# Optimization experiments

Measured on AMD Instinct MI355X. Metric: run time of the kernel, lower is better.

The kernel has to match this reference:

```python
import jax, jax.numpy as jnp
import numpy as np

B, S, D = 2, 2048, 1024
H = 16
HD = D // H  # 64
SCALE = HD ** -0.5
EPS = 1e-12  # F.normalize eps


def _rope_sin_cos(length, half, dtype):
    positions = jnp.arange(length, dtype=dtype)
    freqs = jnp.arange(half, dtype=dtype)
    inv_freq = 1.0 / 10000 ** (freqs / max(1, half))
    theta = jnp.einsum('s,f->sf', positions, inv_freq)  # [S, half]
    return jnp.sin(theta)[None, None], jnp.cos(theta)[None, None]  # [1,1,S,half]


def _rotate(x, sin, cos):
    # x: [B,H,S,HD]; interleaved even/odd rotation
    x_even = x[..., 0::2]
    x_odd = x[..., 1::2]
    r_even = x_even * cos - x_odd * sin
    r_odd = x_even * sin + x_odd * cos
    return jnp.stack([r_even, r_odd], axis=-1).reshape(x.shape)


def setup_inputs() -> dict:
    key = jax.random.key(0)
    k1, k2, k3 = jax.random.split(key, 3)
    tokens = jax.random.normal(k1, (B, S, D), dtype=jnp.float32)
    qkv_w = jax.random.normal(k2, (3 * D, D), dtype=jnp.float32) * (D ** -0.5)
    qkv_b = jnp.zeros((3 * D,), dtype=jnp.float32)
    out_w = jax.random.normal(k3, (D, D), dtype=jnp.float32) * (D ** -0.5)
    out_b = jnp.zeros((D,), dtype=jnp.float32)
    return {"tokens": tokens, "qkv_w": qkv_w, "qkv_b": qkv_b,
            "out_w": out_w, "out_b": out_b}


def reference(tokens, qkv_w, qkv_b, out_w, out_b):
    batch, length, _ = tokens.shape
    qkv = tokens @ qkv_w.T + qkv_b                       # [B,S,3D]
    qkv = qkv.reshape(batch, length, 3, H, HD)
    qkv = jnp.transpose(qkv, (0, 3, 1, 2, 4))            # [B,H,S,3,HD]
    q, k, v = qkv[..., 0, :], qkv[..., 1, :], qkv[..., 2, :]
    sin, cos = _rope_sin_cos(length, HD // 2, q.dtype)
    q = _rotate(q, sin, cos)
    k = _rotate(k, sin, cos)
    # QK L2-normalize (F.normalize: x / max(||x||, eps))
    q = q / jnp.maximum(jnp.linalg.norm(q, axis=-1, keepdims=True), EPS)
    k = k / jnp.maximum(jnp.linalg.norm(k, axis=-1, keepdims=True), EPS)
    scores = jnp.einsum('bhqd,bhkd->bhqk', q, k) * SCALE
    attn = jax.nn.softmax(scores, axis=-1)
    out = jnp.einsum('bhqk,bhkd->bhqd', attn, v)          # [B,H,S,HD]
    out = jnp.transpose(out, (0, 2, 1, 3)).reshape(batch, length, D)
    return out @ out_w.T + out_b
```

## Files before the change

### kernel.cpp

```cpp
#include <hip/hip_runtime.h>
#include <hip/hip_bf16.h>
#include <math.h>

#define B_ 2
#define S_ 2048
#define D_ 1024
#define H_ 16
#define HD_ 64
#define BHS (B_*H_*S_)
#define NROWS (B_*S_)

typedef __attribute__((ext_vector_type(8))) short bf16x8;
typedef __attribute__((ext_vector_type(4))) short bf16x4;
typedef __attribute__((ext_vector_type(4))) float f32x4;
typedef __attribute__((ext_vector_type(4))) int i32x4;

#ifdef __HIP_DEVICE_COMPILE__
#define EXP2(x) __builtin_amdgcn_exp2f(x)
#else
#define EXP2(x) exp2f(x)
#endif

#define MFMA32(a, b, c) __builtin_amdgcn_mfma_f32_16x16x32_bf16(a, b, c, 0, 0, 0)

#define SCALE_LOG2E 0.18033688011112043f

__device__ __forceinline__ short f2bf(float x) {
  __hip_bfloat16 h = __float2bfloat16(x);
  return *reinterpret_cast<short*>(&h);
}
__device__ __forceinline__ int packbf_hu(float lo, float hi) {
  unsigned lb = __float_as_uint(lo) + 0x8000u;
  unsigned hb = __float_as_uint(hi) + 0x8000u;
  return (int)__builtin_amdgcn_perm(hb, lb, 0x07060302u);
}

__device__ __forceinline__ void gload_lds16(const short* g, short* l) {
  __builtin_amdgcn_global_load_lds(
      (const __attribute__((address_space(1))) void*)g,
      (__attribute__((address_space(3))) void*)l, 16, 0, 0);
}

__global__ __launch_bounds__(256) void prep(
    const float* __restrict__ tokens, const float* __restrict__ qkv_w,
    const float* __restrict__ out_w, short* __restrict__ tok_bf,
    short* __restrict__ qkvw_bf, short* __restrict__ outw_bf,
    float* __restrict__ tab) {
  const int i = blockIdx.x * 256 + threadIdx.x;
  const float* src;
  short* dst;
  int j;
  if (i < 524288) {
    src = tokens; dst = tok_bf; j = i;
  } else if (i < 917504) {
    src = qkv_w; dst = qkvw_bf; j = i - 524288;
  } else if (i < 1048576) {
    src = out_w; dst = outw_bf; j = i - 917504;
  } else if (i < 1056768) {
    const int e = (i - 1048576) * 8;
    const int s = e >> 5;
    const int f0 = e & 31;
#pragma unroll
    for (int k = 0; k < 8; k++) {
      const int f = f0 + k;
      const float theta = (float)s * exp2f(-(float)f * 0.41524101186092034f);
      float sn, cs;
      sincosf(theta, &sn, &cs);
      tab[(s * 32 + f) * 2] = sn;
      tab[(s * 32 + f) * 2 + 1] = cs;
    }
    return;
  } else {
    return;
  }
  const float4 a = *(const float4*)(src + (long)j * 8);
  const float4 b = *(const float4*)(src + (long)j * 8 + 4);
  short tmp[8] = {f2bf(a.x), f2bf(a.y), f2bf(a.z), f2bf(a.w),
                  f2bf(b.x), f2bf(b.y), f2bf(b.z), f2bf(b.w)};
  *(bf16x8*)(dst + (long)j * 8) = *(const bf16x8*)tmp;
}

__global__ __launch_bounds__(256) void qkv_mfma(
    const short* __restrict__ A, const short* __restrict__ W,
    const float* __restrict__ bias, const float* __restrict__ tab,
    short* __restrict__ qb, short* __restrict__ kb, short* __restrict__ vtb) {
  __shared__ short smem[12288];
  const int t = threadIdx.x;
  const int w = t >> 6;
  const int lane = t & 63;
  const int col = lane & 15;
  const int quad = lane >> 4;
  const int wm = w >> 1;
  const int wn = w & 1;
  const int bid = blockIdx.x;
  const int xcd = bid & 7;
  const int seq = bid >> 3;
  const int m0 = (seq / 3) * 64;
  const int n0 = (xcd * 3 + seq % 3) * 128;

  f32x4 acc[2][4] = {};

  auto stage = [&](short* As, short* Bs, int k0) {
    {
      const int c = w * 64 + lane;
      const int row = c >> 2;
      const int gseg = (c & 3) ^ (row & 3);
      gload_lds16(&A[(m0 + row) * 1024 + k0 + gseg * 8], As + w * 512);
    }
#pragma unroll
    for (int i = 0; i < 2; i++) {
      const int c0 = i * 256 + w * 64;
      const int c = c0 + lane;
      const int row = c >> 2;
      const int gseg = (c & 3) ^ (row & 3);
      gload_lds16(&W[(n0 + row) * 1024 + k0 + gseg * 8], Bs + c0 * 8);
    }
  };

  auto compute = [&](const short* As, const short* Bs) {
    bf16x8 af[2], bfr[4];
#pragma unroll
    for (int mt = 0; mt < 2; mt++) {
      const int m = wm * 32 + mt * 16 + col;
      af[mt] = *(const bf16x8*)&As[m * 32 + ((quad ^ (m & 3)) * 8)];
    }
#pragma unroll
    for (int nt = 0; nt < 4; nt++) {
      const int n = wn * 64 + nt * 16 + col;
      bfr[nt] = *(const bf16x8*)&Bs[n * 32 + ((quad ^ (n & 3)) * 8)];
    }
#pragma unroll
    for (int mt = 0; mt < 2; mt++)
#pragma unroll
      for (int nt = 0; nt < 4; nt++)
        acc[mt][nt] = MFMA32(af[mt], bfr[nt], acc[mt][nt]);
  };

  short* As0 = smem;
  short* Bs0 = smem + 2048;
  short* As1 = smem + 6144;
  short* Bs1 = smem + 8192;

  stage(As0, Bs0, 0);
  __syncthreads();
  for (int it = 0; it < 16; it++) {
    const int k0 = it * 64;
    stage(As1, Bs1, k0 + 32);
    compute(As0, Bs0);
    __syncthreads();
    if (it < 15) stage(As0, Bs0, k0 + 64);
    compute(As1, Bs1);
    __syncthreads();
  }

  const int j_base = n0 + wn * 64;
  const int c = j_base >> 10;
  const int h = (j_base >> 6) & 15;
  float bi[4];
#pragma unroll
  for (int nt = 0; nt < 4; nt++) bi[nt] = bias[j_base + nt * 16 + col];

  if (c < 2) {
    short* dst = (c == 0) ? qb : kb;
    float* Tf = (float*)smem + w * 1088;
#pragma unroll
    for (int mt = 0; mt < 2; mt++) {
#pragma unroll
      for (int nt = 0; nt < 4; nt++)
#pragma unroll
        for (int r = 0; r < 4; r++)
          Tf[(quad * 4 + r) * 68 + nt * 16 + col] = acc[mt][nt][r] + bi[nt];
#pragma unroll
      for (int p = 0; p < 4; p++) {
        const int rloc = p * 4 + quad;
        const int n = m0 + wm * 32 + mt * 16 + rloc;
        const int bidx = n >> 11;
        const int s = n & 2047;
        const float4 xv = *(const float4*)&Tf[rloc * 68 + col * 4];
        const float4 tc = *(const float4*)&tab[s * 64 + col * 4];
        const float e0 = xv.x * tc.y - xv.y * tc.x;
        const float o0 = xv.x * tc.x + xv.y * tc.y;
        const float e1 = xv.z * tc.w - xv.w * tc.z;
        const float o1 = xv.z * tc.z + xv.w * tc.w;
        float ss = e0 * e0 + o0 * o0 + e1 * e1 + o1 * o1;
        ss += __shfl_xor(ss, 1, 64);
        ss += __shfl_xor(ss, 2, 64);
        ss += __shfl_xor(ss, 4, 64);
        ss += __shfl_xor(ss, 8, 64);
        const float scl = 1.0f / fmaxf(sqrtf(ss), 1e-12f);
        int2 pk;
        pk.x = packbf_hu(e0 * scl, o0 * scl);
        pk.y = packbf_hu(e1 * scl, o1 * scl);
        *(int2*)&dst[((long)(bidx * 16 + h) * 2048 + s) * 64 + col * 4] = pk;
      }
    }
  } else {
    const int bidx = m0 >> 11;
    const int st = (m0 & 2047) >> 6;
    short* vbase = vtb + ((long)(bidx * 16 + h) * 32 + st) * 4096;
#pragma unroll
    for (int mt = 0; mt < 2; mt++)
#pragma unroll
      for (int ntq = 0; ntq < 4; ntq++) {
        int2 pk;
        pk.x = packbf_hu(acc[mt][ntq][0] + bi[ntq], acc[mt][ntq][1] + bi[ntq]);
        pk.y = packbf_hu(acc[mt][ntq][2] + bi[ntq], acc[mt][ntq][3] + bi[ntq]);
        *(int2*)&vbase[(((wm * 2 + mt) * 4 + ntq) * 32 + quad * 8 +
                        (col >> 1)) * 8 + (col & 1) * 4] = pk;
      }
  }
}

__global__ __launch_bounds__(512) void attn_mfma(
    const short* __restrict__ qb,
    const short* __restrict__ kb,
    const short* __restrict__ vt,
    short* __restrict__ ob) {
  __shared__ __align__(16) char smem[65536];
  short* Ks = (short*)smem;
  short* Vs = Ks + 16384;
  const int t = threadIdx.x;
  const int w = t >> 6;
  const int grp = w >> 2;
  const int wl = w & 3;
  const int lane = t & 63;
  const int col = lane & 15;
  const int quad = lane >> 4;
  const int bh = blockIdx.x;
  const int q0 = blockIdx.y * 128;
  const long hb = (long)bh * S_ * 64;
  const short* kg = kb + hb;
  const short* vg = vt + (long)bh * 64 * S_;

  bf16x8 qa[2][2];
#pragma unroll
  for (int mt2 = 0; mt2 < 2; mt2++)
#pragma unroll
    for (int h = 0; h < 2; h++)
      qa[mt2][h] = *(const bf16x8*)&qb[hb +
          (long)(q0 + wl * 32 + mt2 * 16 + col) * 64 + h * 32 + quad * 8];

  const int tt = (wl << 6) | lane;
  int kofs[2];
#pragma unroll
  for (int i = 0; i < 2; i++) {
    const int cc = tt + 256 * i;
    kofs[i] = ((cc >> 7) * 16 + (cc & 15)) * 64 + ((cc >> 6) & 1) * 32 +
              ((cc >> 4) & 3) * 8;
  }

  short* KfL0 = Ks + grp * 4096;
  short* KfL1 = KfL0 + 8192;
  short* VfL0 = Vs + grp * 4096;
  short* VfL1 = VfL0 + 8192;

  f32x4 oacc[2][4] = {};
  f32x4 lacc[2] = {};
  const short oneb = 0x3F80;
  const bf16x8 ones8 = {oneb, oneb, oneb, oneb, oneb, oneb, oneb, oneb};

  auto stage = [&](short* KfL, short* VfL, int kt) {
    const short* kgp = kg + (long)kt * 64;
    const short* vgp = vg + (long)(kt >> 6) * 4096;
#pragma unroll
    for (int i = 0; i < 2; i++) {
      gload_lds16(kgp + kofs[i], KfL + i * 2048 + wl * 512);
      gload_lds16(vgp + (tt + 256 * i) * 8, VfL + i * 2048 + wl * 512);
    }
  };

  auto compute = [&](const short* KfL, const short* VfL) {
#pragma unroll
    for (int ntp = 0; ntp < 2; ntp++) {
      i32x4 pw[2];
#pragma unroll
      for (int half = 0; half < 2; half++) {
        const int nt = ntp * 2 + half;
        const bf16x8 ka0 =
            *(const bf16x8*)&KfL[nt * 1024 + quad * 128 + col * 8];
        const bf16x8 ka1 =
            *(const bf16x8*)&KfL[nt * 1024 + 512 + quad * 128 + col * 8];
#pragma unroll
        for (int mt2 = 0; mt2 < 2; mt2++) {
          f32x4 z = {0.f, 0.f, 0.f, 0.f};
          z = MFMA32(ka0, qa[mt2][0], z);
          z = MFMA32(ka1, qa[mt2][1], z);
          const float e0 = EXP2(z[0] * SCALE_LOG2E);
          const float e1 = EXP2(z[1] * SCALE_LOG2E);
          const float e2 = EXP2(z[2] * SCALE_LOG2E);
          const float e3 = EXP2(z[3] * SCALE_LOG2E);
          if (half == 0) {
            pw[mt2].x = packbf_hu(e0, e1);
            pw[mt2].y = packbf_hu(e2, e3);
          } else {
            pw[mt2].z = packbf_hu(e0, e1);
            pw[mt2].w = packbf_hu(e2, e3);
          }
        }
      }
      const bf16x8 pb0 = __builtin_bit_cast(bf16x8, pw[0]);
      const bf16x8 pb1 = __builtin_bit_cast(bf16x8, pw[1]);
      lacc[0] = MFMA32(ones8, pb0, lacc[0]);
      lacc[1] = MFMA32(ones8, pb1, lacc[1]);
#pragma unroll
      for (int dt = 0; dt < 4; dt++) {
        const bf16x4 v0 = *(const bf16x4*)
            &VfL[((ntp * 2 + 0) * 4 + dt) * 256 + quad * 64 + col * 4];
        const bf16x4 v1 = *(const bf16x4*)
            &VfL[((ntp * 2 + 1) * 4 + dt) * 256 + quad * 64 + col * 4];
        const bf16x8 va = __builtin_shufflevector(v0, v1, 0, 1, 2, 3, 4, 5, 6, 7);
        oacc[0][dt] = MFMA32(va, pb0, oacc[0][dt]);
        oacc[1][dt] = MFMA32(va, pb1, oacc[1][dt]);
      }
    }
  };

  const int base = grp * 1024;
  stage(KfL0, VfL0, base);
  __syncthreads();
  for (int it = 0; it < 8; it++) {
    const int kt0 = base + it * 128;
    stage(KfL1, VfL1, kt0 + 64);
    compute(KfL0, VfL0);
    __syncthreads();
    if (it < 7) stage(KfL0, VfL0, kt0 + 128);
    compute(KfL1, VfL1);
    __syncthreads();
  }

  float* Ocomb = (float*)smem;
  float* lsumC = (float*)(smem + 34816);
  if (grp == 1) {
#pragma unroll
    for (int mt2 = 0; mt2 < 2; mt2++) {
      const int qloc = wl * 32 + mt2 * 16 + col;
      if (quad == 0) lsumC[qloc] = lacc[mt2][0];
#pragma unroll
      for (int dt = 0; dt < 4; dt++)
        *(f32x4*)&Ocomb[qloc * 68 + dt * 16 + quad * 4] = oacc[mt2][dt];
    }
  }
  __syncthreads();
  if (grp == 0) {
#pragma unroll
    for (int mt2 = 0; mt2 < 2; mt2++) {
      const int qloc = wl * 32 + mt2 * 16 + col;
      const float inv = 1.0f / (lacc[mt2][0] + lsumC[qloc]);
      short* orow = ob + hb + (long)(q0 + qloc) * 64;
#pragma unroll
      for (int dt = 0; dt < 4; dt++) {
        const float4 oc = *(const float4*)&Ocomb[qloc * 68 + dt * 16 + quad * 4];
        int2 pk;
        pk.x = packbf_hu((oacc[mt2][dt][0] + oc.x) * inv,
                         (oacc[mt2][dt][1] + oc.y) * inv);
        pk.y = packbf_hu((oacc[mt2][dt][2] + oc.z) * inv,
                         (oacc[mt2][dt][3] + oc.w) * inv);
        *(int2*)&orow[dt * 16 + quad * 4] = pk;
      }
    }
  }
}

__global__ __launch_bounds__(256) void out_mfma(
    const short* __restrict__ O, const short* __restrict__ W,
    const float* __restrict__ bias, float* __restrict__ out) {
  __shared__ short smem[8192];
  const int t = threadIdx.x;
  const int w = t >> 6;
  const int lane = t & 63;
  const int col = lane & 15;
  const int quad = lane >> 4;
  const int wm = w >> 1;
  const int wn = w & 1;
  const int bid = blockIdx.x;
  const int xcd = bid & 7;
  const int seq = bid >> 3;
  const int m0 = (seq >> 1) * 64;
  const int n0 = (xcd * 2 + (seq & 1)) * 64;

  f32x4 acc[2][2] = {};

  auto stage = [&](short* As, short* Bs, int k0) {
    {
      const int c = w * 64 + lane;
      const int row = c >> 2;
      const int gseg = (c & 3) ^ (row & 3);
      const int n = m0 + row;
      const int bidx = n >> 11;
      const int s = n & 2047;
      const int kk = k0 + gseg * 8;
      gload_lds16(&O[((long)(bidx * 16 + (kk >> 6)) * 2048 + s) * 64 + (kk & 63)],
                  As + w * 512);
    }
    {
      const int c = w * 64 + lane;
      const int row = c >> 2;
      const int gseg = (c & 3) ^ (row & 3);
      gload_lds16(&W[(n0 + row) * 1024 + k0 + gseg * 8], Bs + w * 512);
    }
  };

  auto compute = [&](const short* As, const short* Bs) {
    bf16x8 af[2], bfr[2];
#pragma unroll
    for (int mt = 0; mt < 2; mt++) {
      const int m = wm * 32 + mt * 16 + col;
      af[mt] = *(const bf16x8*)&As[m * 32 + ((quad ^ (m & 3)) * 8)];
    }
#pragma unroll
    for (int nt = 0; nt < 2; nt++) {
      const int n = wn * 32 + nt * 16 + col;
      bfr[nt] = *(const bf16x8*)&Bs[n * 32 + ((quad ^ (n & 3)) * 8)];
    }
#pragma unroll
    for (int mt = 0; mt < 2; mt++)
#pragma unroll
      for (int nt = 0; nt < 2; nt++)
        acc[mt][nt] = MFMA32(af[mt], bfr[nt], acc[mt][nt]);
  };

  short* As0 = smem;
  short* Bs0 = smem + 2048;
  short* As1 = smem + 4096;
  short* Bs1 = smem + 6144;

  stage(As0, Bs0, 0);
  __syncthreads();
  for (int it = 0; it < 16; it++) {
    const int k0 = it * 64;
    stage(As1, Bs1, k0 + 32);
    compute(As0, Bs0);
    __syncthreads();
    if (it < 15) stage(As0, Bs0, k0 + 64);
    compute(As1, Bs1);
    __syncthreads();
  }

  float bi[2];
#pragma unroll
  for (int nt = 0; nt < 2; nt++) bi[nt] = bias[n0 + wn * 32 + nt * 16 + col];
#pragma unroll
  for (int mt = 0; mt < 2; mt++) {
#pragma unroll
    for (int r = 0; r < 4; r++) {
      const int n = m0 + wm * 32 + mt * 16 + quad * 4 + r;
#pragma unroll
      for (int nt = 0; nt < 2; nt++)
        out[(long)n * 1024 + n0 + wn * 32 + nt * 16 + col] =
            acc[mt][nt][r] + bi[nt];
    }
  }
}

extern "C" void kernel_launch(void* const* d_in, const int* in_sizes, int n_in,
                              void* d_out, int out_size, void* d_ws,
                              size_t ws_size, hipStream_t stream) {
  const float* tokens = (const float*)d_in[0];
  const float* qkv_w = (const float*)d_in[1];
  const float* qkv_b = (const float*)d_in[2];
  const float* out_w = (const float*)d_in[3];
  const float* out_b = (const float*)d_in[4];
  float* out = (float*)d_out;

  const size_t per = (size_t)BHS * HD_;
  float* tab = (float*)d_ws;
  short* tok_bf = (short*)(tab + 2048 * 64);
  short* qkvw_bf = tok_bf + per;
  short* outw_bf = qkvw_bf + 3 * per / 4;
  short* q_bf = outw_bf + per / 4;
  short* k_bf = q_bf + per;
  short* vt_bf = k_bf + per;
  short* O_bf = vt_bf + per;

  hipLaunchKernelGGL(prep, dim3(4128), dim3(256), 0, stream, tokens, qkv_w,
                     out_w, tok_bf, qkvw_bf, outw_bf, tab);
  hipLaunchKernelGGL(qkv_mfma, dim3(1536), dim3(256), 0, stream, tok_bf,
                     qkvw_bf, qkv_b, tab, q_bf, k_bf, vt_bf);
  hipLaunchKernelGGL(attn_mfma, dim3(B_ * H_, S_ / 128), dim3(512), 0, stream,
                     q_bf, k_bf, vt_bf, O_bf);
  hipLaunchKernelGGL(out_mfma, dim3(1024), dim3(256), 0, stream, O_bf,
                     outw_bf, out_b, out);
}
```

Baseline: 192.3 us.

## Enlarge QKV GEMM tile to 128x128 and change LDS swizzle pattern

```diff
diff --git a/kernel.cpp b/kernel.cpp
--- a/kernel.cpp
+++ b/kernel.cpp
@@ -84,7 +84,7 @@
     const short* __restrict__ A, const short* __restrict__ W,
     const float* __restrict__ bias, const float* __restrict__ tab,
     short* __restrict__ qb, short* __restrict__ kb, short* __restrict__ vtb) {
-  __shared__ short smem[12288];
+  __shared__ short smem[16384];
   const int t = threadIdx.x;
   const int w = t >> 6;
   const int lane = t & 63;
@@ -95,51 +95,53 @@
   const int bid = blockIdx.x;
   const int xcd = bid & 7;
   const int seq = bid >> 3;
-  const int m0 = (seq / 3) * 64;
+  const int m0 = (seq / 3) * 128;
   const int n0 = (xcd * 3 + seq % 3) * 128;
 
-  f32x4 acc[2][4] = {};
+  f32x4 acc[4][4] = {};
 
   auto stage = [&](short* As, short* Bs, int k0) {
-    {
-      const int c = w * 64 + lane;
-      const int row = c >> 2;
-      const int gseg = (c & 3) ^ (row & 3);
-      gload_lds16(&A[(m0 + row) * 1024 + k0 + gseg * 8], As + w * 512);
-    }
 #pragma unroll
     for (int i = 0; i < 2; i++) {
       const int c0 = i * 256 + w * 64;
       const int c = c0 + lane;
       const int row = c >> 2;
-      const int gseg = (c & 3) ^ (row & 3);
+      const int gseg = (c & 3) ^ ((row >> 1) & 3);
+      gload_lds16(&A[(m0 + row) * 1024 + k0 + gseg * 8], As + c0 * 8);
+    }
+#pragma unroll
+    for (int i = 0; i < 2; i++) {
+      const int c0 = i * 256 + w * 64;
+      const int c = c0 + lane;
+      const int row = c >> 2;
+      const int gseg = (c & 3) ^ ((row >> 1) & 3);
       gload_lds16(&W[(n0 + row) * 1024 + k0 + gseg * 8], Bs + c0 * 8);
     }
   };
 
   auto compute = [&](const short* As, const short* Bs) {
-    bf16x8 af[2], bfr[4];
-#pragma unroll
-    for (int mt = 0; mt < 2; mt++) {
-      const int m = wm * 32 + mt * 16 + col;
-      af[mt] = *(const bf16x8*)&As[m * 32 + ((quad ^ (m & 3)) * 8)];
+    bf16x8 af[4], bfr[4];
+#pragma unroll
+    for (int mt = 0; mt < 4; mt++) {
+      const int m = wm * 64 + mt * 16 + col;
+      af[mt] = *(const bf16x8*)&As[m * 32 + ((quad ^ ((m >> 1) & 3)) * 8)];
     }
 #pragma unroll
     for (int nt = 0; nt < 4; nt++) {
       const int n = wn * 64 + nt * 16 + col;
-      bfr[nt] = *(const bf16x8*)&Bs[n * 32 + ((quad ^ (n & 3)) * 8)];
-    }
-#pragma unroll
-    for (int mt = 0; mt < 2; mt++)
+      bfr[nt] = *(const bf16x8*)&Bs[n * 32 + ((quad ^ ((n >> 1) & 3)) * 8)];
+    }
+#pragma unroll
+    for (int mt = 0; mt < 4; mt++)
 #pragma unroll
       for (int nt = 0; nt < 4; nt++)
         acc[mt][nt] = MFMA32(af[mt], bfr[nt], acc[mt][nt]);
   };
 
   short* As0 = smem;
-  short* Bs0 = smem + 2048;
-  short* As1 = smem + 6144;
-  short* Bs1 = smem + 8192;
+  short* Bs0 = smem + 4096;
+  short* As1 = smem + 8192;
+  short* Bs1 = smem + 12288;
 
   stage(As0, Bs0, 0);
   __syncthreads();
@@ -164,7 +166,7 @@
     short* dst = (c == 0) ? qb : kb;
     float* Tf = (float*)smem + w * 1088;
 #pragma unroll
-    for (int mt = 0; mt < 2; mt++) {
+    for (int mt = 0; mt < 4; mt++) {
 #pragma unroll
       for (int nt = 0; nt < 4; nt++)
 #pragma unroll
@@ -173,7 +175,7 @@
 #pragma unroll
       for (int p = 0; p < 4; p++) {
         const int rloc = p * 4 + quad;
-        const int n = m0 + wm * 32 + mt * 16 + rloc;
+        const int n = m0 + wm * 64 + mt * 16 + rloc;
         const int bidx = n >> 11;
         const int s = n & 2047;
         const float4 xv = *(const float4*)&Tf[rloc * 68 + col * 4];
@@ -196,17 +198,17 @@
     }
   } else {
     const int bidx = m0 >> 11;
-    const int st = (m0 & 2047) >> 6;
+    const int st = ((m0 & 2047) >> 6) + wm;
     short* vbase = vtb + ((long)(bidx * 16 + h) * 32 + st) * 4096;
 #pragma unroll
-    for (int mt = 0; mt < 2; mt++)
+    for (int mt = 0; mt < 4; mt++)
 #pragma unroll
       for (int ntq = 0; ntq < 4; ntq++) {
         int2 pk;
         pk.x = packbf_hu(acc[mt][ntq][0] + bi[ntq], acc[mt][ntq][1] + bi[ntq]);
         pk.y = packbf_hu(acc[mt][ntq][2] + bi[ntq], acc[mt][ntq][3] + bi[ntq]);
-        *(int2*)&vbase[(((wm * 2 + mt) * 4 + ntq) * 32 + quad * 8 +
-                        (col >> 1)) * 8 + (col & 1) * 4] = pk;
+        *(int2*)&vbase[((mt * 4 + ntq) * 32 + quad * 8 + (col >> 1)) * 8 +
+                       (col & 1) * 4] = pk;
       }
   }
 }
@@ -384,7 +386,7 @@
     {
       const int c = w * 64 + lane;
       const int row = c >> 2;
-      const int gseg = (c & 3) ^ (row & 3);
+      const int gseg = (c & 3) ^ ((row >> 1) & 3);
       const int n = m0 + row;
       const int bidx = n >> 11;
       const int s = n & 2047;
@@ -395,7 +397,7 @@
     {
       const int c = w * 64 + lane;
       const int row = c >> 2;
-      const int gseg = (c & 3) ^ (row & 3);
+      const int gseg = (c & 3) ^ ((row >> 1) & 3);
       gload_lds16(&W[(n0 + row) * 1024 + k0 + gseg * 8], Bs + w * 512);
     }
   };
@@ -405,12 +407,12 @@
 #pragma unroll
     for (int mt = 0; mt < 2; mt++) {
       const int m = wm * 32 + mt * 16 + col;
-      af[mt] = *(const bf16x8*)&As[m * 32 + ((quad ^ (m & 3)) * 8)];
+      af[mt] = *(const bf16x8*)&As[m * 32 + ((quad ^ ((m >> 1) & 3)) * 8)];
     }
 #pragma unroll
     for (int nt = 0; nt < 2; nt++) {
       const int n = wn * 32 + nt * 16 + col;
-      bfr[nt] = *(const bf16x8*)&Bs[n * 32 + ((quad ^ (n & 3)) * 8)];
+      bfr[nt] = *(const bf16x8*)&Bs[n * 32 + ((quad ^ ((n >> 1) & 3)) * 8)];
     }
 #pragma unroll
     for (int mt = 0; mt < 2; mt++)
@@ -474,7 +476,7 @@
 
   hipLaunchKernelGGL(prep, dim3(4128), dim3(256), 0, stream, tokens, qkv_w,
                      out_w, tok_bf, qkvw_bf, outw_bf, tab);
-  hipLaunchKernelGGL(qkv_mfma, dim3(1536), dim3(256), 0, stream, tok_bf,
+  hipLaunchKernelGGL(qkv_mfma, dim3(768), dim3(256), 0, stream, tok_bf,
                      qkvw_bf, qkv_b, tab, q_bf, k_bf, vt_bf);
   hipLaunchKernelGGL(attn_mfma, dim3(B_ * H_, S_ / 128), dim3(512), 0, stream,
                      q_bf, k_bf, vt_bf, O_bf);
```

Result: faster. 184.4 us (-4.1%).
